# Optimization experiments

Measured on AMD Instinct MI355X. Metric: run time of the kernel, lower is better.

The kernel has to match this reference:

```python
import jax, jax.numpy as jnp
import numpy as np

jax.config.update("jax_enable_x64", True)

POOL = np.array([4.0, 4.0, 4.0], dtype=np.float32)  # pool_size
N, E, D, B = 400_000, 3_200_000, 64, 16


def setup_inputs() -> dict:
    key = jax.random.key(0)
    k1, k2, k3, k4 = jax.random.split(key, 4)
    x = jax.random.normal(k1, (N, D), dtype=jnp.float32)
    pos = jax.random.uniform(k2, (N, 3), dtype=jnp.float32) * 128.0
    batch = jnp.sort(jax.random.randint(k3, (N,), 0, B)).astype(jnp.int64)
    edge_index = jax.random.randint(k4, (E, 2), 0, N).astype(jnp.int64)
    return {"x": x, "pos": pos, "edge_index": edge_index, "batch": batch}


def _voxel_key(pos, batch):
    # torch.div(pos, pool, rounding_mode='floor').long()
    qpos = jnp.floor(pos / jnp.asarray(POOL)).astype(jnp.int64)  # [N,3]
    strides = [int(qpos[:, i].max()) + 1 for i in range(3)]
    k = batch.astype(jnp.int64)
    for i in range(3):
        k = k * strides[i] + qpos[:, i]  # linearized (batch, qx, qy, qz) key
    return k, strides


def reference(x, pos, edge_index, batch):
    keyv, s = _voxel_key(pos, batch)
    ukey, inv = jnp.unique(keyv, return_inverse=True)  # unique voxel keys
    M = int(ukey.shape[0])
    new_batch = ukey // (s[0] * s[1] * s[2])  # recover batch id from key prefix

    # average_positions=True: scatter-mean of pos (include_self=False == pure mean)
    counts = jax.ops.segment_sum(jnp.ones((pos.shape[0],), pos.dtype), inv, num_segments=M)
    pos_mean = jax.ops.segment_sum(pos, inv, num_segments=M) / counts[:, None]

    # scatter-reduce amax of features (every segment non-empty by construction)
    pooled_x = jax.ops.segment_max(x, inv, num_segments=M)

    # remap edges, drop self-loops, dedup, append self-loops for all M nodes
    ei = inv[edge_index]  # [E,2]
    mask = ei[:, 0] != ei[:, 1]
    enc = ei[:, 0].astype(jnp.int64) * M + ei[:, 1].astype(jnp.int64)
    uenc = jnp.unique(enc[mask])
    ei_dedup = jnp.stack([uenc // M, uenc % M], axis=1)
    ar = jnp.arange(M, dtype=ei_dedup.dtype)
    loops = jnp.stack([ar, ar], axis=1)
    ei_out = jnp.concatenate([ei_dedup, loops], axis=0)

    return pooled_x, pos_mean, ei_out, new_batch
```

## Files before the change

kernel.cpp:

```cpp
#include <hip/hip_runtime.h>


#define KSP 524288
#define SCAN_BLOCK 256
#define SCAN_ITEMS 16
#define SCAN_CHUNK 4096
#define NCHUNK (KSP / SCAN_CHUNK)
#define NPART 1024
#define PB 512
#define SCAP2 8192
#define PS_ITERS 16


__global__ void k_qmax(const float* __restrict__ pos, unsigned* hdr, int N) {
  __shared__ unsigned sm[3];
  if (threadIdx.x < 3) sm[threadIdx.x] = 0;
  __syncthreads();
  int i = blockIdx.x * blockDim.x + threadIdx.x;
  if (i < N) {
    int q0 = (int)floorf(pos[3 * i + 0] * 0.25f);
    int q1 = (int)floorf(pos[3 * i + 1] * 0.25f);
    int q2 = (int)floorf(pos[3 * i + 2] * 0.25f);
    atomicMax(&sm[0], (unsigned)q0);
    atomicMax(&sm[1], (unsigned)q1);
    atomicMax(&sm[2], (unsigned)q2);
  }
  __syncthreads();
  if (threadIdx.x < 3) atomicMax(&hdr[threadIdx.x], sm[threadIdx.x]);
}

__global__ void k_keys(const float* __restrict__ pos, const int* __restrict__ batch,
                       const unsigned* __restrict__ hdr, unsigned* __restrict__ key,
                       unsigned* __restrict__ cnt, int N) {
  int i = blockIdx.x * blockDim.x + threadIdx.x;
  if (i >= N) return;
  unsigned s0 = hdr[0] + 1, s1 = hdr[1] + 1, s2 = hdr[2] + 1;
  unsigned q0 = (unsigned)(int)floorf(pos[3 * i + 0] * 0.25f);
  unsigned q1 = (unsigned)(int)floorf(pos[3 * i + 1] * 0.25f);
  unsigned q2 = (unsigned)(int)floorf(pos[3 * i + 2] * 0.25f);
  unsigned k = (((unsigned)batch[i] * s0 + q0) * s1 + q1) * s2 + q2;
  key[i] = k;
  atomicAdd(&cnt[k], 1u);
}

__global__ void scanA(const unsigned* __restrict__ in, unsigned* __restrict__ out,
                      unsigned* __restrict__ chunkSums, int n, int presence) {
  __shared__ unsigned lds[SCAN_BLOCK];
  int tbase = blockIdx.x * SCAN_CHUNK + threadIdx.x * SCAN_ITEMS;
  unsigned vals[SCAN_ITEMS];
  unsigned sum = 0;
  for (int i = 0; i < SCAN_ITEMS; ++i) {
    unsigned v = 0;
    int idx = tbase + i;
    if (idx < n) { v = in[idx]; if (presence) v = v ? 1u : 0u; }
    vals[i] = sum;
    sum += v;
  }
  lds[threadIdx.x] = sum;
  __syncthreads();
  for (int off = 1; off < SCAN_BLOCK; off <<= 1) {
    unsigned t = (threadIdx.x >= (unsigned)off) ? lds[threadIdx.x - off] : 0u;
    __syncthreads();
    lds[threadIdx.x] += t;
    __syncthreads();
  }
  unsigned threadExcl = lds[threadIdx.x] - sum;
  for (int i = 0; i < SCAN_ITEMS; ++i) {
    int idx = tbase + i;
    if (idx < n) out[idx] = threadExcl + vals[i];
  }
  if (threadIdx.x == SCAN_BLOCK - 1) chunkSums[blockIdx.x] = lds[SCAN_BLOCK - 1];
}

__global__ void scanB(unsigned* chunkSums, unsigned* totalDst, int nchunks) {
  __shared__ unsigned lds[1024];
  unsigned v = (threadIdx.x < (unsigned)nchunks) ? chunkSums[threadIdx.x] : 0u;
  lds[threadIdx.x] = v;
  __syncthreads();
  for (int off = 1; off < 1024; off <<= 1) {
    unsigned t = (threadIdx.x >= (unsigned)off) ? lds[threadIdx.x - off] : 0u;
    __syncthreads();
    lds[threadIdx.x] += t;
    __syncthreads();
  }
  if (threadIdx.x < (unsigned)nchunks) chunkSums[threadIdx.x] = lds[threadIdx.x] - v;
  if (threadIdx.x == 0 && totalDst) *totalDst = lds[1023];
}

__global__ void scanC(unsigned* __restrict__ out, unsigned* __restrict__ out2,
                      const unsigned* __restrict__ chunkSums, int n) {
  int idx = blockIdx.x * blockDim.x + threadIdx.x;
  if (idx >= n) return;
  unsigned v = out[idx] + chunkSums[idx / SCAN_CHUNK];
  out[idx] = v;
  if (out2) out2[idx] = v;
}

__global__ void k_scan1024(const unsigned* __restrict__ in, unsigned* __restrict__ outStart,
                           unsigned* __restrict__ outCursor, unsigned* __restrict__ totalDst) {
  __shared__ unsigned lds[NPART];
  unsigned t = threadIdx.x;
  unsigned v = in[t];
  lds[t] = v;
  __syncthreads();
  for (int off = 1; off < NPART; off <<= 1) {
    unsigned x = (t >= (unsigned)off) ? lds[t - off] : 0u;
    __syncthreads();
    lds[t] += x;
    __syncthreads();
  }
  unsigned excl = lds[t] - v;
  outStart[t] = excl;
  if (outCursor) outCursor[t] = excl;
  if (t == NPART - 1) {
    outStart[NPART] = lds[t];
    if (totalDst) *totalDst = lds[t];
  }
}

__global__ void k_ukey(const unsigned* __restrict__ cnt, const unsigned* __restrict__ rank,
                       unsigned* __restrict__ ukeyArr) {
  int k = blockIdx.x * blockDim.x + threadIdx.x;
  if (k >= KSP) return;
  if (cnt[k]) ukeyArr[rank[k]] = (unsigned)k;
}

__global__ void k_scatter(const unsigned* __restrict__ key, const unsigned* __restrict__ rank,
                          unsigned* __restrict__ inv, unsigned* __restrict__ ptCursor,
                          unsigned* __restrict__ ptOrder, int N) {
  int i = blockIdx.x * blockDim.x + threadIdx.x;
  if (i >= N) return;
  unsigned k = key[i];
  inv[i] = rank[k];
  unsigned posn = atomicAdd(&ptCursor[k], 1u);
  ptOrder[posn] = (unsigned)i;
}

__global__ void k_cstart(const unsigned* __restrict__ cnt, const unsigned* __restrict__ rank,
                         const unsigned* __restrict__ ptStart, const unsigned* __restrict__ hdr,
                         unsigned* __restrict__ cStart, int N) {
  int k = blockIdx.x * blockDim.x + threadIdx.x;
  if (k >= KSP) return;
  if (cnt[k]) cStart[rank[k]] = ptStart[k];
  if (k == 0) cStart[hdr[3]] = (unsigned)N;
}

__global__ void __launch_bounds__(256) k_pool(const float4* __restrict__ x4,
                                              const float* __restrict__ pos,
                                              const unsigned* __restrict__ ptOrder,
                                              const unsigned* __restrict__ cStart,
                                              const unsigned* __restrict__ hdr,
                                              float* __restrict__ out) {
  unsigned gtid = blockIdx.x * blockDim.x + threadIdx.x;
  unsigned m = gtid >> 3;
  unsigned l = gtid & 7u;
  unsigned M = hdr[3];
  if (m >= M) return;
  unsigned start = cStart[m];
  unsigned n = cStart[m + 1] - start;
  const float NI = -__builtin_huge_valf();
  float4 a0 = make_float4(NI, NI, NI, NI);
  float4 a1 = a0;
  float psum = 0.0f;
  for (unsigned j = 0; j < n; ++j) {
    unsigned p = ptOrder[start + j];
    float4 v0 = x4[p * 16u + l];
    float4 v1 = x4[p * 16u + 8u + l];
    a0.x = fmaxf(a0.x, v0.x); a0.y = fmaxf(a0.y, v0.y);
    a0.z = fmaxf(a0.z, v0.z); a0.w = fmaxf(a0.w, v0.w);
    a1.x = fmaxf(a1.x, v1.x); a1.y = fmaxf(a1.y, v1.y);
    a1.z = fmaxf(a1.z, v1.z); a1.w = fmaxf(a1.w, v1.w);
    if (l < 3) psum += pos[3u * p + l];
  }
  float4* o4 = (float4*)out;
  o4[m * 16u + l] = a0;
  o4[m * 16u + 8u + l] = a1;
  if (l < 3) {
    unsigned long long O1 = 64ull * M;
    out[O1 + 3ull * m + l] = psum / (float)n;
  }
}

__global__ void __launch_bounds__(256) k_ehist2(const int2* __restrict__ ei,
                                                const unsigned* __restrict__ inv,
                                                unsigned* __restrict__ partCnt, int E, int span) {
  __shared__ unsigned h[NPART];
  for (int i = threadIdx.x; i < NPART; i += 256) h[i] = 0;
  __syncthreads();
  int lo = blockIdx.x * span;
  int hi = min(E, lo + span);
  for (int e = lo + threadIdx.x; e < hi; e += 256) {
    int2 pr = ei[e];
    unsigned a = inv[pr.x], b = inv[pr.y];
    if (a != b) atomicAdd(&h[a >> 9], 1u);
  }
  __syncthreads();
  for (int i = threadIdx.x; i < NPART; i += 256) {
    unsigned v = h[i];
    if (v) atomicAdd(&partCnt[i], v);
  }
}

__global__ void __launch_bounds__(256) k_pscatter(const int2* __restrict__ ei,
                                                  const unsigned* __restrict__ inv,
                                                  unsigned* __restrict__ partCursor,
                                                  unsigned* __restrict__ pStage,
                                                  int E) {
  __shared__ unsigned h[NPART];
  for (int i = threadIdx.x; i < NPART; i += 256) h[i] = 0;
  __syncthreads();
  int lo = blockIdx.x * (256 * PS_ITERS);
  unsigned long long codes[PS_ITERS];
#pragma unroll
  for (int it = 0; it < PS_ITERS; ++it) {
    codes[it] = ~0ull;
    int e = lo + threadIdx.x + it * 256;
    if (e < E) {
      int2 pr = ei[e];
      unsigned a = inv[pr.x], b = inv[pr.y];
      if (a != b) {
        codes[it] = ((unsigned long long)a << 19) | b;
        atomicAdd(&h[a >> 9], 1u);
      }
    }
  }
  __syncthreads();
  for (int i = threadIdx.x; i < NPART; i += 256) {
    unsigned v = h[i];
    h[i] = v ? atomicAdd(&partCursor[i], v) : 0u;
  }
  __syncthreads();
#pragma unroll
  for (int it = 0; it < PS_ITERS; ++it) {
    unsigned long long code = codes[it];
    if (code != ~0ull) {
      unsigned a = (unsigned)(code >> 19);
      unsigned off = atomicAdd(&h[a >> 9], 1u);
      pStage[off] = ((a & 511u) << 19) | ((unsigned)code & 0x7FFFFu);
    }
  }
}

__global__ void __launch_bounds__(256) k_bucket(unsigned* __restrict__ pStage,
                                                const unsigned* __restrict__ partStart,
                                                unsigned* __restrict__ partDistinct) {
  __shared__ unsigned dstL[SCAP2];
  __shared__ unsigned h[PB];
  __shared__ unsigned bbase[PB + 1];
  __shared__ unsigned stmp[256];
  unsigned p = blockIdx.x;
  unsigned s = partStart[p];
  unsigned c = partStart[p + 1] - s;
  unsigned t = threadIdx.x;
  for (int i = t; i < PB; i += 256) h[i] = 0;
  __syncthreads();
  if (c <= SCAP2) {
    const unsigned* src = pStage + s;
    for (unsigned i = t; i < c; i += 256) {
      atomicAdd(&h[src[i] >> 19], 1u);
    }
    __syncthreads();
    {
      unsigned a = h[2 * t], b = h[2 * t + 1], sum = a + b;
      stmp[t] = sum;
      __syncthreads();
      for (int off = 1; off < 256; off <<= 1) {
        unsigned x = (t >= (unsigned)off) ? stmp[t - off] : 0u;
        __syncthreads(); stmp[t] += x; __syncthreads();
      }
      unsigned excl = stmp[t] - sum;
      bbase[2 * t] = excl; bbase[2 * t + 1] = excl + a;
      if (t == 255) bbase[PB] = stmp[255];
    }
    __syncthreads();
    for (int i = t; i < PB; i += 256) h[i] = bbase[i];
    __syncthreads();
    for (unsigned i = t; i < c; i += 256) {
      unsigned code28 = src[i];
      unsigned off = atomicAdd(&h[code28 >> 19], 1u);
      dstL[off] = code28;
    }
    __syncthreads();
    unsigned L = (c + 255) >> 8;
    unsigned vv[32], rr[32];
#pragma unroll
    for (unsigned k = 0; k < 32; ++k) {
      unsigned i = t * L + k;
      if (k < L && i < c) {
        unsigned v = dstL[i];
        unsigned b = v >> 19;
        unsigned blo = bbase[b], bhi = bbase[b + 1];
        unsigned r = blo;
        for (unsigned j = blo; j < bhi; ++j) {
          unsigned u = dstL[j];
          r += (u < v) || (u == v && j < i);
        }
        vv[k] = v; rr[k] = r;
      }
    }
    __syncthreads();
#pragma unroll
    for (unsigned k = 0; k < 32; ++k) {
      unsigned i = t * L + k;
      if (k < L && i < c) dstL[rr[k]] = vv[k];
    }
    __syncthreads();
    unsigned flm = 0, localSum = 0;
#pragma unroll
    for (unsigned k = 0; k < 32; ++k) {
      unsigned i = t * L + k;
      if (k < L && i < c) {
        unsigned v = dstL[i];
        unsigned pv = dstL[i - (i > 0 ? 1u : 0u)];
        unsigned f = (i == 0) | (pv != v);
        flm |= f << k;
        localSum += f;
      }
    }
    stmp[t] = localSum;
    __syncthreads();
    for (int off = 1; off < 256; off <<= 1) {
      unsigned x = (t >= (unsigned)off) ? stmp[t - off] : 0u;
      __syncthreads(); stmp[t] += x; __syncthreads();
    }
    unsigned pos = stmp[t] - localSum;
#pragma unroll
    for (unsigned k = 0; k < 32; ++k) {
      unsigned i = t * L + k;
      if (k < L && i < c && ((flm >> k) & 1u)) {
        pStage[s + pos] = dstL[i];
        ++pos;
      }
    }
    if (t == 255) partDistinct[p] = stmp[255];
  } else if (t == 0) {
    unsigned* a = pStage + s;
    for (unsigned i = 1; i < c; ++i) {
      unsigned v = a[i];
      long long j = (long long)i - 1;
      while (j >= 0 && a[j] > v) { a[j + 1] = a[j]; --j; }
      a[j + 1] = v;
    }
    unsigned d = 0, prev = 0xFFFFFFFFu;
    for (unsigned i = 0; i < c; ++i) {
      unsigned v = a[i];
      if (i == 0 || v != prev) { a[d] = v; ++d; }
      prev = v;
    }
    partDistinct[p] = d;
  }
}

__global__ void __launch_bounds__(256) k_ewriteP(const unsigned* __restrict__ pStage,
                                                 const unsigned* __restrict__ partStart,
                                                 const unsigned* __restrict__ partOut,
                                                 const unsigned* __restrict__ hdr,
                                                 float* __restrict__ out) {
  unsigned p = blockIdx.x;
  unsigned s = partStart[p];
  unsigned rbase = partOut[p];
  unsigned d = partOut[p + 1] - rbase;
  unsigned M = hdr[3];
  unsigned long long O2 = 67ull * M;
  unsigned pbase = p << 9;
  for (unsigned j = threadIdx.x; j < d; j += 256) {
    unsigned code = pStage[s + j];
    unsigned long long row = (unsigned long long)rbase + j;
    out[O2 + 2 * row + 0] = (float)(pbase | (code >> 19));
    out[O2 + 2 * row + 1] = (float)(code & 0x7FFFFu);
  }
}

__global__ void k_final(const unsigned* __restrict__ ukeyArr, const unsigned* __restrict__ hdr,
                        float* __restrict__ out) {
  unsigned m = blockIdx.x * blockDim.x + threadIdx.x;
  unsigned M = hdr[3];
  if (m >= M) return;
  unsigned Ed = hdr[5];
  unsigned long long O2 = 67ull * M;
  unsigned long long row = (unsigned long long)Ed + m;
  float fm = (float)m;
  out[O2 + 2 * row + 0] = fm;
  out[O2 + 2 * row + 1] = fm;
  unsigned s0 = hdr[0] + 1, s1 = hdr[1] + 1, s2 = hdr[2] + 1;
  unsigned vol = s0 * s1 * s2;
  unsigned long long O3 = O2 + 2ull * (Ed + M);
  out[O3 + m] = (float)(ukeyArr[m] / vol);
}

extern "C" void kernel_launch(void* const* d_in, const int* in_sizes, int n_in,
                              void* d_out, int out_size, void* d_ws, size_t ws_size,
                              hipStream_t stream) {
  const float* x = (const float*)d_in[0];
  const float* pos = (const float*)d_in[1];
  const int* ei = (const int*)d_in[2];
  const int* batch = (const int*)d_in[3];
  float* out = (float*)d_out;
  int N = in_sizes[3];
  int E = in_sizes[2] / 2;

  unsigned* ws = (unsigned*)d_ws;
  unsigned* hdr          = ws;
  unsigned* cnt          = ws + 64;
  unsigned* partCnt      = cnt + KSP;
  unsigned* partDistinct = partCnt + NPART;
  unsigned* rank         = partDistinct + NPART;
  unsigned* ukeyArr      = rank + KSP;
  unsigned* partStart    = ukeyArr + KSP;
  unsigned* partCursor   = partStart + NPART + 2;
  unsigned* partOut      = partCursor + NPART;
  unsigned* chunkSums    = partOut + NPART + 2;
  unsigned* key          = chunkSums + 1024;
  unsigned* inv          = key + N;
  unsigned* pS32         = inv + ((N + 1) & ~1);
  unsigned* pStage       = pS32;
  unsigned* ptStart  = pS32;
  unsigned* ptCursor = pS32 + KSP;
  unsigned* ptOrder  = pS32 + 2 * KSP;
  unsigned* cStart   = ptCursor;

  hipMemsetAsync(ws, 0, (size_t)(64 + KSP + 2 * NPART) * 4, stream);

  const int B = 256;
  int gN = (N + B - 1) / B;
  int gK = (KSP + B - 1) / B;
  int gP = (int)(((long long)N * 8 + B - 1) / B);
  int ebH = 2048;
  int spanH = (E + ebH - 1) / ebH;
  int ebS = (E + 256 * PS_ITERS - 1) / (256 * PS_ITERS);

  k_qmax<<<gN, B, 0, stream>>>(pos, hdr, N);
  k_keys<<<gN, B, 0, stream>>>(pos, batch, hdr, key, cnt, N);

  scanA<<<NCHUNK, SCAN_BLOCK, 0, stream>>>(cnt, rank, chunkSums, KSP, 1);
  scanB<<<1, 1024, 0, stream>>>(chunkSums, &hdr[3], NCHUNK);
  scanC<<<gK, B, 0, stream>>>(rank, nullptr, chunkSums, KSP);

  scanA<<<NCHUNK, SCAN_BLOCK, 0, stream>>>(cnt, ptStart, chunkSums, KSP, 0);
  scanB<<<1, 1024, 0, stream>>>(chunkSums, &hdr[6], NCHUNK);
  scanC<<<gK, B, 0, stream>>>(ptStart, ptCursor, chunkSums, KSP);

  k_ukey<<<gK, B, 0, stream>>>(cnt, rank, ukeyArr);
  k_scatter<<<gN, B, 0, stream>>>(key, rank, inv, ptCursor, ptOrder, N);
  k_cstart<<<gK, B, 0, stream>>>(cnt, rank, ptStart, hdr, cStart, N);
  k_pool<<<gP, B, 0, stream>>>((const float4*)x, pos, ptOrder, cStart, hdr, out);

  const int2* ei2 = (const int2*)ei;
  k_ehist2<<<ebH, 256, 0, stream>>>(ei2, inv, partCnt, E, spanH);
  k_scan1024<<<1, NPART, 0, stream>>>(partCnt, partStart, partCursor, &hdr[4]);
  k_pscatter<<<ebS, 256, 0, stream>>>(ei2, inv, partCursor, pStage, E);
  k_bucket<<<NPART, 256, 0, stream>>>(pStage, partStart, partDistinct);
  k_scan1024<<<1, NPART, 0, stream>>>(partDistinct, partOut, nullptr, &hdr[5]);
  k_ewriteP<<<NPART, 256, 0, stream>>>(pStage, partStart, partOut, hdr, out);
  k_final<<<gK, B, 0, stream>>>(ukeyArr, hdr, out);

  (void)n_in; (void)ws_size;
}
```

Before: 520.8 us.

## Fuse dual key scans, merge cStart into ukey, double edge partitions

The rank (presence) and point-start (count) exclusive scans over the key space are merged into one three-kernel pass instead of two. The cStart build is folded into k_ukey, and the scatter now uses ptStart directly as its cursor, which removes one kernel and one KSP-sized copy. The edge partitioning moves from 1024 partitions of 512 rows to 2048 partitions of 256 rows, halving per-bucket shared capacity and the per-thread register arrays in k_bucket. Buckets that exceed the smaller capacity would take the fallback path more often.

```diff
diff --git a/kernel.cpp b/kernel.cpp
--- a/kernel.cpp
+++ b/kernel.cpp
@@ -6,9 +6,10 @@
 #define SCAN_ITEMS 16
 #define SCAN_CHUNK 4096
 #define NCHUNK (KSP / SCAN_CHUNK)
-#define NPART 1024
-#define PB 512
-#define SCAP2 8192
+#define NPART 2048
+#define PSHIFT 8
+#define PB 256
+#define SCAP2 4096
 #define PS_ITERS 16
 
 
@@ -43,106 +44,118 @@
   atomicAdd(&cnt[k], 1u);
 }
 
-__global__ void scanA(const unsigned* __restrict__ in, unsigned* __restrict__ out,
-                      unsigned* __restrict__ chunkSums, int n, int presence) {
-  __shared__ unsigned lds[SCAN_BLOCK];
+__global__ void scanA2(const unsigned* __restrict__ in, unsigned* __restrict__ outRank,
+                       unsigned* __restrict__ outStart, unsigned* __restrict__ chunkP,
+                       unsigned* __restrict__ chunkC, int n) {
+  __shared__ unsigned ldsP[SCAN_BLOCK];
+  __shared__ unsigned ldsC[SCAN_BLOCK];
   int tbase = blockIdx.x * SCAN_CHUNK + threadIdx.x * SCAN_ITEMS;
-  unsigned vals[SCAN_ITEMS];
-  unsigned sum = 0;
+  unsigned valsP[SCAN_ITEMS], valsC[SCAN_ITEMS];
+  unsigned sp = 0, sc = 0;
   for (int i = 0; i < SCAN_ITEMS; ++i) {
     unsigned v = 0;
     int idx = tbase + i;
-    if (idx < n) { v = in[idx]; if (presence) v = v ? 1u : 0u; }
-    vals[i] = sum;
-    sum += v;
-  }
-  lds[threadIdx.x] = sum;
+    if (idx < n) v = in[idx];
+    valsP[i] = sp; valsC[i] = sc;
+    sp += v ? 1u : 0u;
+    sc += v;
+  }
+  ldsP[threadIdx.x] = sp; ldsC[threadIdx.x] = sc;
   __syncthreads();
   for (int off = 1; off < SCAN_BLOCK; off <<= 1) {
-    unsigned t = (threadIdx.x >= (unsigned)off) ? lds[threadIdx.x - off] : 0u;
-    __syncthreads();
-    lds[threadIdx.x] += t;
-    __syncthreads();
-  }
-  unsigned threadExcl = lds[threadIdx.x] - sum;
+    unsigned tp = (threadIdx.x >= (unsigned)off) ? ldsP[threadIdx.x - off] : 0u;
+    unsigned tc = (threadIdx.x >= (unsigned)off) ? ldsC[threadIdx.x - off] : 0u;
+    __syncthreads();
+    ldsP[threadIdx.x] += tp; ldsC[threadIdx.x] += tc;
+    __syncthreads();
+  }
+  unsigned exP = ldsP[threadIdx.x] - sp;
+  unsigned exC = ldsC[threadIdx.x] - sc;
   for (int i = 0; i < SCAN_ITEMS; ++i) {
     int idx = tbase + i;
-    if (idx < n) out[idx] = threadExcl + vals[i];
-  }
-  if (threadIdx.x == SCAN_BLOCK - 1) chunkSums[blockIdx.x] = lds[SCAN_BLOCK - 1];
-}
-
-__global__ void scanB(unsigned* chunkSums, unsigned* totalDst, int nchunks) {
-  __shared__ unsigned lds[1024];
-  unsigned v = (threadIdx.x < (unsigned)nchunks) ? chunkSums[threadIdx.x] : 0u;
-  lds[threadIdx.x] = v;
-  __syncthreads();
-  for (int off = 1; off < 1024; off <<= 1) {
-    unsigned t = (threadIdx.x >= (unsigned)off) ? lds[threadIdx.x - off] : 0u;
-    __syncthreads();
-    lds[threadIdx.x] += t;
-    __syncthreads();
-  }
-  if (threadIdx.x < (unsigned)nchunks) chunkSums[threadIdx.x] = lds[threadIdx.x] - v;
-  if (threadIdx.x == 0 && totalDst) *totalDst = lds[1023];
-}
-
-__global__ void scanC(unsigned* __restrict__ out, unsigned* __restrict__ out2,
-                      const unsigned* __restrict__ chunkSums, int n) {
+    if (idx < n) { outRank[idx] = exP + valsP[i]; outStart[idx] = exC + valsC[i]; }
+  }
+  if (threadIdx.x == SCAN_BLOCK - 1) {
+    chunkP[blockIdx.x] = ldsP[SCAN_BLOCK - 1];
+    chunkC[blockIdx.x] = ldsC[SCAN_BLOCK - 1];
+  }
+}
+
+__global__ void scanB2(unsigned* chunkP, unsigned* chunkC, unsigned* mDst) {
+  __shared__ unsigned lp[NCHUNK];
+  __shared__ unsigned lc[NCHUNK];
+  unsigned t = threadIdx.x;
+  unsigned vp = chunkP[t], vc = chunkC[t];
+  lp[t] = vp; lc[t] = vc;
+  __syncthreads();
+  for (int off = 1; off < NCHUNK; off <<= 1) {
+    unsigned xp = (t >= (unsigned)off) ? lp[t - off] : 0u;
+    unsigned xc = (t >= (unsigned)off) ? lc[t - off] : 0u;
+    __syncthreads();
+    lp[t] += xp; lc[t] += xc;
+    __syncthreads();
+  }
+  chunkP[t] = lp[t] - vp;
+  chunkC[t] = lc[t] - vc;
+  if (t == NCHUNK - 1 && mDst) *mDst = lp[NCHUNK - 1];
+}
+
+__global__ void scanC2(unsigned* __restrict__ rank, unsigned* __restrict__ ptStart,
+                       const unsigned* __restrict__ chunkP, const unsigned* __restrict__ chunkC,
+                       int n) {
   int idx = blockIdx.x * blockDim.x + threadIdx.x;
   if (idx >= n) return;
-  unsigned v = out[idx] + chunkSums[idx / SCAN_CHUNK];
-  out[idx] = v;
-  if (out2) out2[idx] = v;
-}
-
-__global__ void k_scan1024(const unsigned* __restrict__ in, unsigned* __restrict__ outStart,
-                           unsigned* __restrict__ outCursor, unsigned* __restrict__ totalDst) {
-  __shared__ unsigned lds[NPART];
+  int ch = idx / SCAN_CHUNK;
+  rank[idx] += chunkP[ch];
+  ptStart[idx] += chunkC[ch];
+}
+
+__global__ void k_scanP(const unsigned* __restrict__ in, unsigned* __restrict__ outStart,
+                        unsigned* __restrict__ outCursor, unsigned* __restrict__ totalDst) {
+  __shared__ unsigned lds[1024];
   unsigned t = threadIdx.x;
-  unsigned v = in[t];
-  lds[t] = v;
-  __syncthreads();
-  for (int off = 1; off < NPART; off <<= 1) {
+  unsigned a = in[2 * t], b = in[2 * t + 1];
+  unsigned sum = a + b;
+  lds[t] = sum;
+  __syncthreads();
+  for (int off = 1; off < 1024; off <<= 1) {
     unsigned x = (t >= (unsigned)off) ? lds[t - off] : 0u;
     __syncthreads();
     lds[t] += x;
     __syncthreads();
   }
-  unsigned excl = lds[t] - v;
-  outStart[t] = excl;
-  if (outCursor) outCursor[t] = excl;
-  if (t == NPART - 1) {
-    outStart[NPART] = lds[t];
-    if (totalDst) *totalDst = lds[t];
+  unsigned excl = lds[t] - sum;
+  outStart[2 * t] = excl;
+  outStart[2 * t + 1] = excl + a;
+  if (outCursor) { outCursor[2 * t] = excl; outCursor[2 * t + 1] = excl + a; }
+  if (t == 1023) {
+    outStart[NPART] = lds[1023];
+    if (totalDst) *totalDst = lds[1023];
   }
 }
 
 __global__ void k_ukey(const unsigned* __restrict__ cnt, const unsigned* __restrict__ rank,
-                       unsigned* __restrict__ ukeyArr) {
+                       const unsigned* __restrict__ ptStart, const unsigned* __restrict__ hdr,
+                       unsigned* __restrict__ ukeyArr, unsigned* __restrict__ cStart, int N) {
   int k = blockIdx.x * blockDim.x + threadIdx.x;
   if (k >= KSP) return;
-  if (cnt[k]) ukeyArr[rank[k]] = (unsigned)k;
+  if (cnt[k]) {
+    unsigned r = rank[k];
+    ukeyArr[r] = (unsigned)k;
+    cStart[r] = ptStart[k];
+  }
+  if (k == 0) cStart[hdr[3]] = (unsigned)N;
 }
 
 __global__ void k_scatter(const unsigned* __restrict__ key, const unsigned* __restrict__ rank,
-                          unsigned* __restrict__ inv, unsigned* __restrict__ ptCursor,
+                          unsigned* __restrict__ inv, unsigned* __restrict__ ptStart,
                           unsigned* __restrict__ ptOrder, int N) {
   int i = blockIdx.x * blockDim.x + threadIdx.x;
   if (i >= N) return;
   unsigned k = key[i];
   inv[i] = rank[k];
-  unsigned posn = atomicAdd(&ptCursor[k], 1u);
+  unsigned posn = atomicAdd(&ptStart[k], 1u);
   ptOrder[posn] = (unsigned)i;
-}
-
-__global__ void k_cstart(const unsigned* __restrict__ cnt, const unsigned* __restrict__ rank,
-                         const unsigned* __restrict__ ptStart, const unsigned* __restrict__ hdr,
-                         unsigned* __restrict__ cStart, int N) {
-  int k = blockIdx.x * blockDim.x + threadIdx.x;
-  if (k >= KSP) return;
-  if (cnt[k]) cStart[rank[k]] = ptStart[k];
-  if (k == 0) cStart[hdr[3]] = (unsigned)N;
 }
 
 __global__ void __launch_bounds__(256) k_pool(const float4* __restrict__ x4,
@@ -192,7 +205,7 @@
   for (int e = lo + threadIdx.x; e < hi; e += 256) {
     int2 pr = ei[e];
     unsigned a = inv[pr.x], b = inv[pr.y];
-    if (a != b) atomicAdd(&h[a >> 9], 1u);
+    if (a != b) atomicAdd(&h[a >> PSHIFT], 1u);
   }
   __syncthreads();
   for (int i = threadIdx.x; i < NPART; i += 256) {
@@ -220,7 +233,7 @@
       unsigned a = inv[pr.x], b = inv[pr.y];
       if (a != b) {
         codes[it] = ((unsigned long long)a << 19) | b;
-        atomicAdd(&h[a >> 9], 1u);
+        atomicAdd(&h[a >> PSHIFT], 1u);
       }
     }
   }
@@ -235,8 +248,8 @@
     unsigned long long code = codes[it];
     if (code != ~0ull) {
       unsigned a = (unsigned)(code >> 19);
-      unsigned off = atomicAdd(&h[a >> 9], 1u);
-      pStage[off] = ((a & 511u) << 19) | ((unsigned)code & 0x7FFFFu);
+      unsigned off = atomicAdd(&h[a >> PSHIFT], 1u);
+      pStage[off] = ((a & (PB - 1u)) << 19) | ((unsigned)code & 0x7FFFFu);
     }
   }
 }
@@ -252,39 +265,36 @@
   unsigned s = partStart[p];
   unsigned c = partStart[p + 1] - s;
   unsigned t = threadIdx.x;
-  for (int i = t; i < PB; i += 256) h[i] = 0;
+  h[t] = 0;
   __syncthreads();
   if (c <= SCAP2) {
     const unsigned* src = pStage + s;
-    for (unsigned i = t; i < c; i += 256) {
-      atomicAdd(&h[src[i] >> 19], 1u);
-    }
+    for (unsigned i = t; i < c; i += 256) atomicAdd(&h[src[i] >> 19], 1u);
     __syncthreads();
     {
-      unsigned a = h[2 * t], b = h[2 * t + 1], sum = a + b;
-      stmp[t] = sum;
+      unsigned v = h[t];
+      stmp[t] = v;
       __syncthreads();
       for (int off = 1; off < 256; off <<= 1) {
         unsigned x = (t >= (unsigned)off) ? stmp[t - off] : 0u;
         __syncthreads(); stmp[t] += x; __syncthreads();
       }
-      unsigned excl = stmp[t] - sum;
-      bbase[2 * t] = excl; bbase[2 * t + 1] = excl + a;
+      bbase[t] = stmp[t] - v;
       if (t == 255) bbase[PB] = stmp[255];
     }
     __syncthreads();
-    for (int i = t; i < PB; i += 256) h[i] = bbase[i];
+    h[t] = bbase[t];
     __syncthreads();
     for (unsigned i = t; i < c; i += 256) {
-      unsigned code28 = src[i];
-      unsigned off = atomicAdd(&h[code28 >> 19], 1u);
-      dstL[off] = code28;
+      unsigned code = src[i];
+      unsigned off = atomicAdd(&h[code >> 19], 1u);
+      dstL[off] = code;
     }
     __syncthreads();
     unsigned L = (c + 255) >> 8;
-    unsigned vv[32], rr[32];
-#pragma unroll
-    for (unsigned k = 0; k < 32; ++k) {
+    unsigned vv[16], rr[16];
+#pragma unroll
+    for (unsigned k = 0; k < 16; ++k) {
       unsigned i = t * L + k;
       if (k < L && i < c) {
         unsigned v = dstL[i];
@@ -300,14 +310,14 @@
     }
     __syncthreads();
 #pragma unroll
-    for (unsigned k = 0; k < 32; ++k) {
+    for (unsigned k = 0; k < 16; ++k) {
       unsigned i = t * L + k;
       if (k < L && i < c) dstL[rr[k]] = vv[k];
     }
     __syncthreads();
     unsigned flm = 0, localSum = 0;
 #pragma unroll
-    for (unsigned k = 0; k < 32; ++k) {
+    for (unsigned k = 0; k < 16; ++k) {
       unsigned i = t * L + k;
       if (k < L && i < c) {
         unsigned v = dstL[i];
@@ -325,7 +335,7 @@
     }
     unsigned pos = stmp[t] - localSum;
 #pragma unroll
-    for (unsigned k = 0; k < 32; ++k) {
+    for (unsigned k = 0; k < 16; ++k) {
       unsigned i = t * L + k;
       if (k < L && i < c && ((flm >> k) & 1u)) {
         pStage[s + pos] = dstL[i];
@@ -362,7 +372,7 @@
   unsigned d = partOut[p + 1] - rbase;
   unsigned M = hdr[3];
   unsigned long long O2 = 67ull * M;
-  unsigned pbase = p << 9;
+  unsigned pbase = p << PSHIFT;
   for (unsigned j = threadIdx.x; j < d; j += 256) {
     unsigned code = pStage[s + j];
     unsigned long long row = (unsigned long long)rbase + j;
@@ -406,18 +416,18 @@
   unsigned* partDistinct = partCnt + NPART;
   unsigned* rank         = partDistinct + NPART;
   unsigned* ukeyArr      = rank + KSP;
-  unsigned* partStart    = ukeyArr + KSP;
+  unsigned* cStart       = ukeyArr + KSP;
+  unsigned* partStart    = cStart + KSP + 2;
   unsigned* partCursor   = partStart + NPART + 2;
   unsigned* partOut      = partCursor + NPART;
-  unsigned* chunkSums    = partOut + NPART + 2;
-  unsigned* key          = chunkSums + 1024;
+  unsigned* chunkP       = partOut + NPART + 2;
+  unsigned* chunkC       = chunkP + 1024;
+  unsigned* key          = chunkC + 1024;
   unsigned* inv          = key + N;
   unsigned* pS32         = inv + ((N + 1) & ~1);
   unsigned* pStage       = pS32;
   unsigned* ptStart  = pS32;
-  unsigned* ptCursor = pS32 + KSP;
-  unsigned* ptOrder  = pS32 + 2 * KSP;
-  unsigned* cStart   = ptCursor;
+  unsigned* ptOrder  = pS32 + KSP;
 
   hipMemsetAsync(ws, 0, (size_t)(64 + KSP + 2 * NPART) * 4, stream);
 
@@ -432,25 +442,20 @@
   k_qmax<<<gN, B, 0, stream>>>(pos, hdr, N);
   k_keys<<<gN, B, 0, stream>>>(pos, batch, hdr, key, cnt, N);
 
-  scanA<<<NCHUNK, SCAN_BLOCK, 0, stream>>>(cnt, rank, chunkSums, KSP, 1);
-  scanB<<<1, 1024, 0, stream>>>(chunkSums, &hdr[3], NCHUNK);
-  scanC<<<gK, B, 0, stream>>>(rank, nullptr, chunkSums, KSP);
-
-  scanA<<<NCHUNK, SCAN_BLOCK, 0, stream>>>(cnt, ptStart, chunkSums, KSP, 0);
-  scanB<<<1, 1024, 0, stream>>>(chunkSums, &hdr[6], NCHUNK);
-  scanC<<<gK, B, 0, stream>>>(ptStart, ptCursor, chunkSums, KSP);
-
-  k_ukey<<<gK, B, 0, stream>>>(cnt, rank, ukeyArr);
-  k_scatter<<<gN, B, 0, stream>>>(key, rank, inv, ptCursor, ptOrder, N);
-  k_cstart<<<gK, B, 0, stream>>>(cnt, rank, ptStart, hdr, cStart, N);
+  scanA2<<<NCHUNK, SCAN_BLOCK, 0, stream>>>(cnt, rank, ptStart, chunkP, chunkC, KSP);
+  scanB2<<<1, NCHUNK, 0, stream>>>(chunkP, chunkC, &hdr[3]);
+  scanC2<<<gK, B, 0, stream>>>(rank, ptStart, chunkP, chunkC, KSP);
+
+  k_ukey<<<gK, B, 0, stream>>>(cnt, rank, ptStart, hdr, ukeyArr, cStart, N);
+  k_scatter<<<gN, B, 0, stream>>>(key, rank, inv, ptStart, ptOrder, N);
   k_pool<<<gP, B, 0, stream>>>((const float4*)x, pos, ptOrder, cStart, hdr, out);
 
   const int2* ei2 = (const int2*)ei;
   k_ehist2<<<ebH, 256, 0, stream>>>(ei2, inv, partCnt, E, spanH);
-  k_scan1024<<<1, NPART, 0, stream>>>(partCnt, partStart, partCursor, &hdr[4]);
+  k_scanP<<<1, 1024, 0, stream>>>(partCnt, partStart, partCursor, &hdr[4]);
   k_pscatter<<<ebS, 256, 0, stream>>>(ei2, inv, partCursor, pStage, E);
   k_bucket<<<NPART, 256, 0, stream>>>(pStage, partStart, partDistinct);
-  k_scan1024<<<1, NPART, 0, stream>>>(partDistinct, partOut, nullptr, &hdr[5]);
+  k_scanP<<<1, 1024, 0, stream>>>(partDistinct, partOut, nullptr, &hdr[5]);
   k_ewriteP<<<NPART, 256, 0, stream>>>(pStage, partStart, partOut, hdr, out);
   k_final<<<gK, B, 0, stream>>>(ukeyArr, hdr, out);
 
```

Measured after the change: 493.0 us. 5.3% less time.
